# Performance work log

Measured on AMD Instinct MI355X. Metric: run time of the kernel, lower is better.

## Reference

```python
import jax, jax.numpy as jnp
import numpy as np


def setup_inputs() -> dict:
    key = jax.random.key(0)
    k1, k2 = jax.random.split(key)
    B, H, W = 16, 1024, 1024
    NB = 20
    preds = jax.random.randint(k1, (B, H, W), 0, NB, dtype=jnp.int32)
    targets = jax.random.randint(k2, (B, H, W), 0, NB, dtype=jnp.int32)
    return {"preds": preds, "targets": targets, "nb_class": NB, "smooth": 1}


def reference(preds, targets, nb_class, smooth):
    # Single-pass histogram formulation of the per-class IoU loop:
    #   intersection[c] = #{pred==c and target==c}
    #   union[c]        = #{pred==c} + #{target==c} - intersection[c]
    p = preds.reshape(-1)
    t = targets.reshape(-1)
    pred_count = jnp.bincount(p, length=nb_class).astype(jnp.float32)
    target_count = jnp.bincount(t, length=nb_class).astype(jnp.float32)
    # pixels where pred==target contribute to intersection of that class
    match = p == t
    intersection = jnp.bincount(jnp.where(match, p, nb_class), length=nb_class + 1)[:nb_class].astype(jnp.float32)
    union = pred_count + target_count - intersection
    s = jnp.float32(smooth)
    iou_per_class = (intersection + s) / (union + s)  # [nb_class]
    mIoU = iou_per_class.mean()
    return 1.0 - mIoU
```

## Files before the change

### kernel.cpp

```cpp
#include <hip/hip_runtime.h>
#include <hip/hip_bf16.h>


#define NB      20
#define NKEY    (NB * NB)
#define NCOPY   32
#define BLK     256
#define GRID_H  512
#define PSTRIDE 64

__device__ __forceinline__ void dma16(const void* g, void* l) {
    __builtin_amdgcn_global_load_lds(
        (const __attribute__((address_space(1))) unsigned*)g,
        (__attribute__((address_space(3))) unsigned*)l, 16, 0, 0);
}

__device__ __forceinline__ void process_pix(int p, int t, unsigned* hist_cp) {
    atomicAdd(&hist_cp[(p * NB + t) * NCOPY], 1u);
}

__device__ __forceinline__ void process_vec(int4 pv, int4 tv, unsigned* hist_cp) {
    process_pix(pv.x, tv.x, hist_cp);
    process_pix(pv.y, tv.y, hist_cp);
    process_pix(pv.z, tv.z, hist_cp);
    process_pix(pv.w, tv.w, hist_cp);
}

__global__ __launch_bounds__(BLK) void miou_hist_kernel(
        const int4* __restrict__ preds, const int4* __restrict__ targs,
        unsigned* __restrict__ partials, int n4, int full_iters) {
    __shared__ unsigned s_hist[NKEY * NCOPY];
    __shared__ int4 s_p[2][BLK];
    __shared__ int4 s_t[2][BLK];
    const int tid  = threadIdx.x;
    const int wid  = tid >> 6;
    const int lane = tid & 63;

    for (int k = tid; k < NKEY * NCOPY; k += BLK) s_hist[k] = 0u;
    __syncthreads();

    unsigned* hist_cp = &s_hist[tid & (NCOPY - 1)];
    const int CHUNK = gridDim.x * BLK;
    const int base  = blockIdx.x * BLK + tid;

    if (full_iters >= 2) {
        dma16(&preds[base],         &s_p[0][wid * 64]);
        dma16(&targs[base],         &s_t[0][wid * 64]);
        dma16(&preds[base + CHUNK], &s_p[1][wid * 64]);
        dma16(&targs[base + CHUNK], &s_t[1][wid * 64]);

        for (int j = 0; j < full_iters - 1; ++j) {
            const int slot = j & 1;
            asm volatile("s_waitcnt vmcnt(2)" ::: "memory");
            int4 pv = s_p[slot][wid * 64 + lane];
            int4 tv = s_t[slot][wid * 64 + lane];
            asm volatile("s_waitcnt lgkmcnt(0)" ::: "memory");
            if (j + 2 < full_iters) {
                dma16(&preds[base + (j + 2) * CHUNK], &s_p[slot][wid * 64]);
                dma16(&targs[base + (j + 2) * CHUNK], &s_t[slot][wid * 64]);
            }
            process_vec(pv, tv, hist_cp);
        }
        {
            const int slot = (full_iters - 1) & 1;
            asm volatile("s_waitcnt vmcnt(0)" ::: "memory");
            int4 pv = s_p[slot][wid * 64 + lane];
            int4 tv = s_t[slot][wid * 64 + lane];
            process_vec(pv, tv, hist_cp);
        }
    }
    for (int i = base + full_iters * CHUNK; i < n4; i += CHUNK) {
        int4 pv = preds[i];
        int4 tv = targs[i];
        process_vec(pv, tv, hist_cp);
    }
    __syncthreads();

    unsigned* dst = &partials[(size_t)blockIdx.x * PSTRIDE];
    for (int c = wid; c < NB; c += (BLK / 64)) {
        unsigned pcs = 0;
        #pragma unroll
        for (int k = 0; k < 640; k += 64) pcs += s_hist[c * 640 + k + lane];

        unsigned tcs = 0;
        {
            const int copy = lane & 31;
            const int p0   = lane >> 5;
            #pragma unroll
            for (int p = 0; p < NB; p += 2)
                tcs += s_hist[(p + p0) * 640 + c * 32 + copy];
        }
        unsigned ics = (lane < 32) ? s_hist[c * 21 * 32 + lane] : 0u;

        #pragma unroll
        for (int off = 32; off > 0; off >>= 1) {
            pcs += __shfl_xor(pcs, off);
            tcs += __shfl_xor(tcs, off);
            ics += __shfl_xor(ics, off);
        }
        if (lane == 0) {
            dst[c]          = pcs;
            dst[NB + c]     = tcs;
            dst[2 * NB + c] = ics;
        }
    }
}

__global__ __launch_bounds__(1024) void miou_reduce_kernel(
        const unsigned* __restrict__ partials, int nblocks,
        const int* __restrict__ nb_ptr, const int* __restrict__ smooth_ptr,
        float* __restrict__ out) {
    __shared__ unsigned s_tot[PSTRIDE];
    if (threadIdx.x < PSTRIDE) s_tot[threadIdx.x] = 0u;
    __syncthreads();

    const int col4 = threadIdx.x & 15;
    const int seg  = threadIdx.x >> 4;
    const int4* p4 = (const int4*)partials;

    unsigned ax = 0, ay = 0, az = 0, aw = 0;
    #pragma unroll 8
    for (int r = seg; r < nblocks; r += 64) {
        int4 v = p4[r * 16 + col4];
        ax += (unsigned)v.x; ay += (unsigned)v.y;
        az += (unsigned)v.z; aw += (unsigned)v.w;
    }
    atomicAdd(&s_tot[col4 * 4 + 0], ax);
    atomicAdd(&s_tot[col4 * 4 + 1], ay);
    atomicAdd(&s_tot[col4 * 4 + 2], az);
    atomicAdd(&s_tot[col4 * 4 + 3], aw);
    __syncthreads();

    if (threadIdx.x == 0) {
        const int   nb = *nb_ptr;
        const float s  = (float)(*smooth_ptr);
        float acc_iou = 0.0f;
        for (int c = 0; c < nb && c < NB; ++c) {
            float pc    = (float)s_tot[c];
            float tc    = (float)s_tot[NB + c];
            float inter = (float)s_tot[2 * NB + c];
            float uni   = pc + tc - inter;
            acc_iou += (inter + s) / (uni + s);
        }
        out[0] = 1.0f - acc_iou / (float)nb;
    }
}

extern "C" void kernel_launch(void* const* d_in, const int* in_sizes, int n_in,
                              void* d_out, int out_size, void* d_ws, size_t ws_size,
                              hipStream_t stream) {
    const int4* preds      = (const int4*)d_in[0];
    const int4* targs      = (const int4*)d_in[1];
    const int*  nb_ptr     = (const int*)d_in[2];
    const int*  smooth_ptr = (const int*)d_in[3];
    float*      out        = (float*)d_out;

    int n  = in_sizes[0];
    int n4 = n >> 2;

    unsigned* partials = (unsigned*)d_ws;

    int grid = GRID_H;
    int max_grid = (n4 + BLK - 1) / BLK;
    if (grid > max_grid) grid = max_grid;
    size_t need_per_block = PSTRIDE * sizeof(unsigned);
    if ((size_t)grid * need_per_block > ws_size)
        grid = (int)(ws_size / need_per_block);

    int chunk = grid * BLK;
    int full  = (chunk > 0) ? (n4 / chunk) : 0;
    if (full < 2) full = 0;

    miou_hist_kernel<<<grid, BLK, 0, stream>>>(preds, targs, partials, n4, full);
    miou_reduce_kernel<<<1, 1024, 0, stream>>>(partials, grid, nb_ptr, smooth_ptr, out);
}
```

Measured before the change: 32.69 us.

## Deepen LDS DMA pipeline to four slots, shrink histogram copies, enlarge grid

```diff
diff --git a/kernel.cpp b/kernel.cpp
--- a/kernel.cpp
+++ b/kernel.cpp
@@ -4,9 +4,10 @@
 
 #define NB      20
 #define NKEY    (NB * NB)
-#define NCOPY   32
+#define NCOPY   8
 #define BLK     256
-#define GRID_H  512
+#define NSLOT   4
+#define GRID_H  768
 #define PSTRIDE 64
 
 __device__ __forceinline__ void dma16(const void* g, void* l) {
@@ -30,8 +31,8 @@
         const int4* __restrict__ preds, const int4* __restrict__ targs,
         unsigned* __restrict__ partials, int n4, int full_iters) {
     __shared__ unsigned s_hist[NKEY * NCOPY];
-    __shared__ int4 s_p[2][BLK];
-    __shared__ int4 s_t[2][BLK];
+    __shared__ int4 s_p[NSLOT][BLK];
+    __shared__ int4 s_t[NSLOT][BLK];
     const int tid  = threadIdx.x;
     const int wid  = tid >> 6;
     const int lane = tid & 63;
@@ -43,54 +44,55 @@
     const int CHUNK = gridDim.x * BLK;
     const int base  = blockIdx.x * BLK + tid;
 
-    if (full_iters >= 2) {
-        dma16(&preds[base],         &s_p[0][wid * 64]);
-        dma16(&targs[base],         &s_t[0][wid * 64]);
-        dma16(&preds[base + CHUNK], &s_p[1][wid * 64]);
-        dma16(&targs[base + CHUNK], &s_t[1][wid * 64]);
+#define STEP(J, VM) do {                                              \
+    const int slot_ = (J) & (NSLOT - 1);                              \
+    asm volatile("s_waitcnt vmcnt(" #VM ")" ::: "memory");            \
+    int4 pv_ = s_p[slot_][wid * 64 + lane];                           \
+    int4 tv_ = s_t[slot_][wid * 64 + lane];                           \
+    asm volatile("s_waitcnt lgkmcnt(0)" ::: "memory");                \
+    if ((J) + NSLOT < full_iters) {                                   \
+        dma16(&preds[base + ((J) + NSLOT) * CHUNK], &s_p[slot_][wid * 64]); \
+        dma16(&targs[base + ((J) + NSLOT) * CHUNK], &s_t[slot_][wid * 64]); \
+    }                                                                 \
+    process_vec(pv_, tv_, hist_cp);                                   \
+} while (0)
 
-        for (int j = 0; j < full_iters - 1; ++j) {
-            const int slot = j & 1;
-            asm volatile("s_waitcnt vmcnt(2)" ::: "memory");
-            int4 pv = s_p[slot][wid * 64 + lane];
-            int4 tv = s_t[slot][wid * 64 + lane];
-            asm volatile("s_waitcnt lgkmcnt(0)" ::: "memory");
-            if (j + 2 < full_iters) {
-                dma16(&preds[base + (j + 2) * CHUNK], &s_p[slot][wid * 64]);
-                dma16(&targs[base + (j + 2) * CHUNK], &s_t[slot][wid * 64]);
-            }
-            process_vec(pv, tv, hist_cp);
+    if (full_iters >= NSLOT) {
+        #pragma unroll
+        for (int s = 0; s < NSLOT; ++s) {
+            dma16(&preds[base + s * CHUNK], &s_p[s][wid * 64]);
+            dma16(&targs[base + s * CHUNK], &s_t[s][wid * 64]);
         }
-        {
-            const int slot = (full_iters - 1) & 1;
-            asm volatile("s_waitcnt vmcnt(0)" ::: "memory");
-            int4 pv = s_p[slot][wid * 64 + lane];
-            int4 tv = s_t[slot][wid * 64 + lane];
-            process_vec(pv, tv, hist_cp);
-        }
+        int j = 0;
+        for (; j < full_iters - (NSLOT - 1); ++j) STEP(j, 6);
+        STEP(j, 4); ++j;
+        STEP(j, 2); ++j;
+        STEP(j, 0);
     }
     for (int i = base + full_iters * CHUNK; i < n4; i += CHUNK) {
         int4 pv = preds[i];
         int4 tv = targs[i];
         process_vec(pv, tv, hist_cp);
     }
+#undef STEP
     __syncthreads();
 
     unsigned* dst = &partials[(size_t)blockIdx.x * PSTRIDE];
     for (int c = wid; c < NB; c += (BLK / 64)) {
         unsigned pcs = 0;
-        #pragma unroll
-        for (int k = 0; k < 640; k += 64) pcs += s_hist[c * 640 + k + lane];
+        pcs += s_hist[c * 160 + lane];
+        pcs += s_hist[c * 160 + 64 + lane];
+        if (lane < 32) pcs += s_hist[c * 160 + 128 + lane];
 
         unsigned tcs = 0;
         {
-            const int copy = lane & 31;
-            const int p0   = lane >> 5;
-            #pragma unroll
-            for (int p = 0; p < NB; p += 2)
-                tcs += s_hist[(p + p0) * 640 + c * 32 + copy];
+            const int p  = lane >> 3;
+            const int cp = lane & 7;
+            tcs += s_hist[(p * NB + c) * NCOPY + cp];
+            tcs += s_hist[((p + 8) * NB + c) * NCOPY + cp];
+            if (p < 4) tcs += s_hist[((p + 16) * NB + c) * NCOPY + cp];
         }
-        unsigned ics = (lane < 32) ? s_hist[c * 21 * 32 + lane] : 0u;
+        unsigned ics = (lane < NCOPY) ? s_hist[c * 21 * NCOPY + lane] : 0u;
 
         #pragma unroll
         for (int off = 32; off > 0; off >>= 1) {
@@ -169,7 +171,7 @@
 
     int chunk = grid * BLK;
     int full  = (chunk > 0) ? (n4 / chunk) : 0;
-    if (full < 2) full = 0;
+    if (full < NSLOT) full = 0;
 
     miou_hist_kernel<<<grid, BLK, 0, stream>>>(preds, targs, partials, n4, full);
     miou_reduce_kernel<<<1, 1024, 0, stream>>>(partials, grid, nb_ptr, smooth_ptr, out);
```

New measurement: 34.46 us. +5.4%, slower.

## Replace LDS double-buffer with fully unrolled register loads over larger grid

Applied to the files above, without the earlier changes.

```diff
diff --git a/kernel.cpp b/kernel.cpp
--- a/kernel.cpp
+++ b/kernel.cpp
@@ -4,34 +4,35 @@
 
 #define NB      20
 #define NKEY    (NB * NB)
-#define NCOPY   32
+#define NCOPY   16
 #define BLK     256
-#define GRID_H  512
+#define GRID_H  2048
 #define PSTRIDE 64
+#define FAST_ITERS 8
 
-__device__ __forceinline__ void dma16(const void* g, void* l) {
-    __builtin_amdgcn_global_load_lds(
-        (const __attribute__((address_space(1))) unsigned*)g,
-        (__attribute__((address_space(3))) unsigned*)l, 16, 0, 0);
+typedef int v4i __attribute__((ext_vector_type(4)));
+
+__device__ __forceinline__ v4i ld16(const v4i* p) {
+    v4i r;
+    asm volatile("global_load_dwordx4 %0, %1, off" : "=&v"(r) : "v"(p));
+    return r;
 }
 
-__device__ __forceinline__ void process_pix(int p, int t, unsigned* hist_cp) {
-    atomicAdd(&hist_cp[(p * NB + t) * NCOPY], 1u);
-}
+#define SB0() __builtin_amdgcn_sched_barrier(0)
+#define WAITPAIR(N, a, b) \
+    asm volatile("s_waitcnt vmcnt(" #N ")" : "+v"(a), "+v"(b) :: "memory")
 
-__device__ __forceinline__ void process_vec(int4 pv, int4 tv, unsigned* hist_cp) {
-    process_pix(pv.x, tv.x, hist_cp);
-    process_pix(pv.y, tv.y, hist_cp);
-    process_pix(pv.z, tv.z, hist_cp);
-    process_pix(pv.w, tv.w, hist_cp);
+__device__ __forceinline__ void consume4(v4i p, v4i t, unsigned* hist_cp) {
+    atomicAdd(&hist_cp[(p.x * NB + t.x) * NCOPY], 1u);
+    atomicAdd(&hist_cp[(p.y * NB + t.y) * NCOPY], 1u);
+    atomicAdd(&hist_cp[(p.z * NB + t.z) * NCOPY], 1u);
+    atomicAdd(&hist_cp[(p.w * NB + t.w) * NCOPY], 1u);
 }
 
 __global__ __launch_bounds__(BLK) void miou_hist_kernel(
-        const int4* __restrict__ preds, const int4* __restrict__ targs,
-        unsigned* __restrict__ partials, int n4, int full_iters) {
+        const v4i* __restrict__ preds, const v4i* __restrict__ targs,
+        unsigned* __restrict__ partials, int n4, int fast) {
     __shared__ unsigned s_hist[NKEY * NCOPY];
-    __shared__ int4 s_p[2][BLK];
-    __shared__ int4 s_t[2][BLK];
     const int tid  = threadIdx.x;
     const int wid  = tid >> 6;
     const int lane = tid & 63;
@@ -40,39 +41,34 @@
     __syncthreads();
 
     unsigned* hist_cp = &s_hist[tid & (NCOPY - 1)];
-    const int CHUNK = gridDim.x * BLK;
-    const int base  = blockIdx.x * BLK + tid;
+    const int stride = gridDim.x * BLK;
+    const int base   = blockIdx.x * BLK + tid;
 
-    if (full_iters >= 2) {
-        dma16(&preds[base],         &s_p[0][wid * 64]);
-        dma16(&targs[base],         &s_t[0][wid * 64]);
-        dma16(&preds[base + CHUNK], &s_p[1][wid * 64]);
-        dma16(&targs[base + CHUNK], &s_t[1][wid * 64]);
-
-        for (int j = 0; j < full_iters - 1; ++j) {
-            const int slot = j & 1;
-            asm volatile("s_waitcnt vmcnt(2)" ::: "memory");
-            int4 pv = s_p[slot][wid * 64 + lane];
-            int4 tv = s_t[slot][wid * 64 + lane];
-            asm volatile("s_waitcnt lgkmcnt(0)" ::: "memory");
-            if (j + 2 < full_iters) {
-                dma16(&preds[base + (j + 2) * CHUNK], &s_p[slot][wid * 64]);
-                dma16(&targs[base + (j + 2) * CHUNK], &s_t[slot][wid * 64]);
-            }
-            process_vec(pv, tv, hist_cp);
+    if (fast) {
+        const v4i* pp = preds + base;
+        const v4i* tp = targs + base;
+        v4i p0 = ld16(pp);               v4i t0 = ld16(tp);
+        v4i p1 = ld16(pp + 1 * stride);  v4i t1 = ld16(tp + 1 * stride);
+        v4i p2 = ld16(pp + 2 * stride);  v4i t2 = ld16(tp + 2 * stride);
+        v4i p3 = ld16(pp + 3 * stride);  v4i t3 = ld16(tp + 3 * stride);
+        v4i p4 = ld16(pp + 4 * stride);  v4i t4 = ld16(tp + 4 * stride);
+        v4i p5 = ld16(pp + 5 * stride);  v4i t5 = ld16(tp + 5 * stride);
+        v4i p6 = ld16(pp + 6 * stride);  v4i t6 = ld16(tp + 6 * stride);
+        v4i p7 = ld16(pp + 7 * stride);  v4i t7 = ld16(tp + 7 * stride);
+        WAITPAIR(14, p0, t0); SB0(); consume4(p0, t0, hist_cp);
+        WAITPAIR(12, p1, t1); SB0(); consume4(p1, t1, hist_cp);
+        WAITPAIR(10, p2, t2); SB0(); consume4(p2, t2, hist_cp);
+        WAITPAIR(8,  p3, t3); SB0(); consume4(p3, t3, hist_cp);
+        WAITPAIR(6,  p4, t4); SB0(); consume4(p4, t4, hist_cp);
+        WAITPAIR(4,  p5, t5); SB0(); consume4(p5, t5, hist_cp);
+        WAITPAIR(2,  p6, t6); SB0(); consume4(p6, t6, hist_cp);
+        WAITPAIR(0,  p7, t7); SB0(); consume4(p7, t7, hist_cp);
+    } else {
+        for (int i = base; i < n4; i += stride) {
+            v4i pv = preds[i];
+            v4i tv = targs[i];
+            consume4(pv, tv, hist_cp);
         }
-        {
-            const int slot = (full_iters - 1) & 1;
-            asm volatile("s_waitcnt vmcnt(0)" ::: "memory");
-            int4 pv = s_p[slot][wid * 64 + lane];
-            int4 tv = s_t[slot][wid * 64 + lane];
-            process_vec(pv, tv, hist_cp);
-        }
-    }
-    for (int i = base + full_iters * CHUNK; i < n4; i += CHUNK) {
-        int4 pv = preds[i];
-        int4 tv = targs[i];
-        process_vec(pv, tv, hist_cp);
     }
     __syncthreads();
 
@@ -80,17 +76,17 @@
     for (int c = wid; c < NB; c += (BLK / 64)) {
         unsigned pcs = 0;
         #pragma unroll
-        for (int k = 0; k < 640; k += 64) pcs += s_hist[c * 640 + k + lane];
+        for (int k = 0; k < 5; ++k) pcs += s_hist[c * 320 + k * 64 + lane];
 
         unsigned tcs = 0;
         {
-            const int copy = lane & 31;
-            const int p0   = lane >> 5;
+            const int cp = lane & 15;
+            const int pb = lane >> 4;
             #pragma unroll
-            for (int p = 0; p < NB; p += 2)
-                tcs += s_hist[(p + p0) * 640 + c * 32 + copy];
+            for (int rep = 0; rep < 5; ++rep)
+                tcs += s_hist[((pb + rep * 4) * NB + c) * NCOPY + cp];
         }
-        unsigned ics = (lane < 32) ? s_hist[c * 21 * 32 + lane] : 0u;
+        unsigned ics = (lane < NCOPY) ? s_hist[(c * 21) * NCOPY + lane] : 0u;
 
         #pragma unroll
         for (int off = 32; off > 0; off >>= 1) {
@@ -149,8 +145,8 @@
 extern "C" void kernel_launch(void* const* d_in, const int* in_sizes, int n_in,
                               void* d_out, int out_size, void* d_ws, size_t ws_size,
                               hipStream_t stream) {
-    const int4* preds      = (const int4*)d_in[0];
-    const int4* targs      = (const int4*)d_in[1];
+    const v4i*  preds      = (const v4i*)d_in[0];
+    const v4i*  targs      = (const v4i*)d_in[1];
     const int*  nb_ptr     = (const int*)d_in[2];
     const int*  smooth_ptr = (const int*)d_in[3];
     float*      out        = (float*)d_out;
@@ -167,10 +163,8 @@
     if ((size_t)grid * need_per_block > ws_size)
         grid = (int)(ws_size / need_per_block);
 
-    int chunk = grid * BLK;
-    int full  = (chunk > 0) ? (n4 / chunk) : 0;
-    if (full < 2) full = 0;
+    int fast = (grid == GRID_H) && (n4 == FAST_ITERS * GRID_H * BLK);
 
-    miou_hist_kernel<<<grid, BLK, 0, stream>>>(preds, targs, partials, n4, full);
+    miou_hist_kernel<<<grid, BLK, 0, stream>>>(preds, targs, partials, n4, fast);
     miou_reduce_kernel<<<1, 1024, 0, stream>>>(partials, grid, nb_ptr, smooth_ptr, out);
 }
```

Result: slower. 45.25 us (+38.4%).
